# Kernel tuning notes

Hardware: AMD Instinct MI355X
Metric: run time of the kernel (lower is better)

Reference implementation:

```python
import jax, jax.numpy as jnp
import numpy as np

N = 100000
E = 1600000
IN_CH, HID_CH, OUT_CH = 128, 64, 32


def setup_inputs() -> dict:
    key = jax.random.key(0)
    ks = jax.random.split(key, 6)
    x = jax.random.normal(ks[0], (N, IN_CH), dtype=jnp.float32)
    ei = jax.random.randint(ks[1], (2, E), 0, N, dtype=jnp.int64)
    W1 = jax.random.normal(ks[2], (IN_CH, HID_CH), dtype=jnp.float32) * 0.05
    b1 = jax.random.normal(ks[3], (HID_CH,), dtype=jnp.float32) * 0.05
    W2 = jax.random.normal(ks[4], (HID_CH, OUT_CH), dtype=jnp.float32) * 0.05
    b2 = jax.random.normal(ks[5], (OUT_CH,), dtype=jnp.float32) * 0.05
    return {"x": x, "ei": ei, "W1": W1, "b1": b1, "W2": W2, "b2": b2}


def gcn_layer(x, sa, da, n):
    # degree with self-loops already appended in sa/da
    deg = jax.ops.segment_sum(jnp.ones((sa.shape[0],), x.dtype), da, num_segments=n)
    prod = deg[sa] * deg[da]
    norm = jnp.where(prod > 0, jax.lax.rsqrt(prod), 0.0)  # (deg_s*deg_d)^-0.5, inf->0
    msg = x[sa] * norm[:, None]            # [E+N, C] gather + scale
    return jax.ops.segment_sum(msg, da, num_segments=n)  # scatter_add


def reference(x, ei, W1, b1, W2, b2):
    n = x.shape[0]
    loop = jnp.arange(n, dtype=ei.dtype)
    sa = jnp.concatenate([ei[0], loop])
    da = jnp.concatenate([ei[1], loop])
    h = gcn_layer(x @ W1 + b1, sa, da, n)
    h = jax.nn.relu(h)
    # dropout: eval mode (training=False) -> identity
    return gcn_layer(h @ W2 + b2, sa, da, n)
```

## Files before the change

kernel.cpp:

```cpp
#include <hip/hip_runtime.h>

#define NN 100000
#define NE 1600000
#define IN_CH 128
#define HID_CH 64
#define OUT_CH 32
#define NB2 98
#define CHUNKA 8192
#define NBLKA ((NE + CHUNKA - 1) / CHUNKA)

typedef unsigned short ushort_t;
typedef _Float16 half2_t __attribute__((ext_vector_type(2)));

__device__ inline ushort_t f2bf(float f) {
    union { float f; unsigned u; } v; v.f = f;
    unsigned r = v.u + 0x7fff + ((v.u >> 16) & 1);
    return (ushort_t)(r >> 16);
}
__device__ inline float blo(unsigned u) {
    union { unsigned x; float f; } v; v.x = u << 16; return v.f;
}
__device__ inline float bhi(unsigned u) {
    union { unsigned x; float f; } v; v.x = u & 0xffff0000u; return v.f;
}
__device__ inline unsigned pkh(float a, float b) {
    union { half2_t h; unsigned u; } v;
    v.h[0] = (_Float16)a; v.h[1] = (_Float16)b;
    return v.u;
}
__device__ inline half2_t u2h(unsigned u) {
    union { unsigned u; half2_t h; } v; v.u = u; return v.h;
}
__device__ inline float fdot2(unsigned a, unsigned b, float c) {
#if __has_builtin(__builtin_amdgcn_fdot2)
    return __builtin_amdgcn_fdot2(u2h(a), u2h(b), c, false);
#else
    half2_t ha = u2h(a), hb = u2h(b);
    return c + (float)ha[0] * (float)hb[0] + (float)ha[1] * (float)hb[1];
#endif
}

__global__ __launch_bounds__(256) void k_bhist(const int* __restrict__ da,
                                               int* __restrict__ bcnt,
                                               int* __restrict__ bhall) {
    __shared__ int hist[4][NB2];
    int t = threadIdx.x, w = t >> 6;
    for (int i = t; i < 4 * NB2; i += 256) ((int*)hist)[i] = 0;
    __syncthreads();
    int base = blockIdx.x * CHUNKA;
    for (int i = 0; i < CHUNKA; i += 256) {
        int e = base + i + t;
        if (e < NE) atomicAdd(&hist[w][da[e] >> 10], 1);
    }
    __syncthreads();
    if (t < NB2) {
        int c = hist[0][t] + hist[1][t] + hist[2][t] + hist[3][t];
        bhall[blockIdx.x * NB2 + t] = c;
        if (c) atomicAdd(&bcnt[t], c);
    }
}

__global__ __launch_bounds__(128) void k_bscan(const int* __restrict__ bcnt,
                                               int* __restrict__ bbase,
                                               int* __restrict__ bcur,
                                               int* __restrict__ rowptr) {
    __shared__ int lds[128];
    int t = threadIdx.x;
    int v = (t < NB2) ? bcnt[t] : 0;
    lds[t] = v;
    __syncthreads();
    for (int off = 1; off < 128; off <<= 1) {
        int x = (t >= off) ? lds[t - off] : 0;
        __syncthreads();
        lds[t] += x;
        __syncthreads();
    }
    int excl = lds[t] - v;
    if (t < NB2) { bbase[t] = excl; bcur[t] = excl; }
    if (t == 0) { bbase[NB2] = NE; rowptr[NN] = NE; }
}

__global__ __launch_bounds__(256) void k_bfill(const int* __restrict__ sa,
                                               const int* __restrict__ da,
                                               const int* __restrict__ bhall,
                                               int* __restrict__ bcur,
                                               unsigned* __restrict__ ebuf) {
    __shared__ int lcur[NB2];
    int t = threadIdx.x;
    if (t < NB2) {
        int c = bhall[blockIdx.x * NB2 + t];
        lcur[t] = c ? atomicAdd(&bcur[t], c) : 0;
    }
    __syncthreads();
    int base = blockIdx.x * CHUNKA;
    for (int i = 0; i < CHUNKA; i += 256) {
        int e = base + i + t;
        if (e < NE) {
            int d = da[e];
            int p = atomicAdd(&lcur[d >> 10], 1);
            ebuf[p] = ((unsigned)sa[e] << 10) | (unsigned)(d & 1023);
        }
    }
}

__global__ __launch_bounds__(256) void k_bfine(const unsigned* __restrict__ ebuf,
                                               const int* __restrict__ bbase,
                                               int* __restrict__ rowptr,
                                               float* __restrict__ rs,
                                               int* __restrict__ col) {
    __shared__ int cnt[1024];
    __shared__ int scn[256];
    __shared__ int cur[256];
    int b = blockIdx.x, t = threadIdx.x;
    int B = b >> 2, slice = b & 3;
    int beg = bbase[B], end = bbase[B + 1];
    *(int4*)&cnt[t * 4] = make_int4(0, 0, 0, 0);
    __syncthreads();
    for (int i = beg + t; i < end; i += 256) atomicAdd(&cnt[ebuf[i] & 1023], 1);
    __syncthreads();
    int4 v4 = *(int4*)&cnt[t * 4];
    int s = v4.x + v4.y + v4.z + v4.w;
    scn[t] = s;
    __syncthreads();
    for (int off = 1; off < 256; off <<= 1) {
        int x = (t >= off) ? scn[t - off] : 0;
        __syncthreads();
        scn[t] += x;
        __syncthreads();
    }
    int excl = scn[t] - s;
    if ((t >> 6) == slice) {
        int p0 = excl;
        int p1 = p0 + v4.x;
        int p2 = p1 + v4.y;
        int p3 = p2 + v4.z;
        int dlo = t * 4;
        int n = B * 1024 + dlo;
        int ci = dlo - slice * 256;
        if (n + 0 < NN) { rowptr[n + 0] = beg + p0; rs[n + 0] = rsqrtf((float)(v4.x + 1)); cur[ci + 0] = beg + p0; }
        if (n + 1 < NN) { rowptr[n + 1] = beg + p1; rs[n + 1] = rsqrtf((float)(v4.y + 1)); cur[ci + 1] = beg + p1; }
        if (n + 2 < NN) { rowptr[n + 2] = beg + p2; rs[n + 2] = rsqrtf((float)(v4.z + 1)); cur[ci + 2] = beg + p2; }
        if (n + 3 < NN) { rowptr[n + 3] = beg + p3; rs[n + 3] = rsqrtf((float)(v4.w + 1)); cur[ci + 3] = beg + p3; }
    }
    __syncthreads();
    int slo = slice * 256;
    for (int i = beg + t; i < end; i += 256) {
        unsigned w = ebuf[i];
        int dlo = (int)(w & 1023);
        if ((dlo >> 8) == slice) {
            int pos = atomicAdd(&cur[dlo - slo], 1);
            col[pos] = (int)(w >> 10);
        }
    }
}

#define SWZU1(n, k2) ((n) * 64 + ((k2) ^ ((((n) & 7)) << 2)))
#define SWZ2(n, k) ((n) * 64 + ((k) ^ ((((n) & 7)) << 2)))

__global__ __launch_bounds__(256, 4) void k_gemm1(
    const float* __restrict__ x, const float* __restrict__ W1,
    const float* __restrict__ b1, const float* __restrict__ rs,
    ushort_t* __restrict__ xsb) {
    __shared__ unsigned xth[64 * 64];
    __shared__ unsigned w1h[64 * 64];
    int t = threadIdx.x;
    int base = blockIdx.x * 64;

#pragma unroll
    for (int i = 0; i < 8; ++i) {
        int flat = i * 1024 + t * 4;
        int node = flat >> 7, k0 = flat & 127;
        int gn = base + node;
        float4 v = make_float4(0.f, 0.f, 0.f, 0.f);
        if (gn < NN) v = *(const float4*)(x + (size_t)gn * IN_CH + k0);
        uint2 pk;
        pk.x = pkh(v.x, v.y);
        pk.y = pkh(v.z, v.w);
        *(uint2*)&xth[SWZU1(node, k0 >> 1)] = pk;
    }
#pragma unroll
    for (int i = 0; i < 16; ++i) {
        int idx = i * 256 + t;
        int k2 = idx >> 6, c = idx & 63;
        float f0 = W1[(2 * k2) * 64 + c];
        float f1 = W1[(2 * k2 + 1) * 64 + c];
        w1h[idx] = pkh(f0, f1);
    }
    __syncthreads();

    int tn = t & 15, tc = t >> 4;
    int c0 = tc * 4;
    float acc[4][4];
#pragma unroll
    for (int a = 0; a < 4; ++a)
#pragma unroll
        for (int b = 0; b < 4; ++b) acc[a][b] = 0.f;

    for (int k2 = 0; k2 < 64; k2 += 2) {
        uint2 xu[4];
#pragma unroll
        for (int jn = 0; jn < 4; ++jn)
            xu[jn] = *(uint2*)&xth[SWZU1(tn + jn * 16, k2)];
        uint4 w0 = *(uint4*)&w1h[(k2 + 0) * 64 + c0];
        uint4 w1 = *(uint4*)&w1h[(k2 + 1) * 64 + c0];
        unsigned wq0[4] = {w0.x, w0.y, w0.z, w0.w};
        unsigned wq1[4] = {w1.x, w1.y, w1.z, w1.w};
#pragma unroll
        for (int jn = 0; jn < 4; ++jn)
#pragma unroll
            for (int jc = 0; jc < 4; ++jc) {
                acc[jn][jc] = fdot2(xu[jn].x, wq0[jc], acc[jn][jc]);
                acc[jn][jc] = fdot2(xu[jn].y, wq1[jc], acc[jn][jc]);
            }
    }

    float4 bb = *(const float4*)&b1[c0];
#pragma unroll
    for (int jn = 0; jn < 4; ++jn) {
        int gn = base + tn + jn * 16;
        if (gn < NN) {
            float r = rs[gn];
            uint2 pk;
            pk.x = (unsigned)f2bf((acc[jn][0] + bb.x) * r) |
                   ((unsigned)f2bf((acc[jn][1] + bb.y) * r) << 16);
            pk.y = (unsigned)f2bf((acc[jn][2] + bb.z) * r) |
                   ((unsigned)f2bf((acc[jn][3] + bb.w) * r) << 16);
            *(uint2*)&xsb[(size_t)gn * HID_CH + c0] = pk;
        }
    }
}

#define ADD8(v) do { \
    a0 += blo((v).x); a1 += bhi((v).x); a2 += blo((v).y); a3 += bhi((v).y); \
    a4 += blo((v).z); a5 += bhi((v).z); a6 += blo((v).w); a7 += bhi((v).w); } while (0)

__global__ __launch_bounds__(256) void k_agg1(
    const int* __restrict__ rowptr, const int* __restrict__ col,
    const ushort_t* __restrict__ xsb, const float* __restrict__ rs,
    ushort_t* __restrict__ hb) {
    int gid = blockIdx.x * blockDim.x + threadIdx.x;
    int n = gid >> 6;
    if (n >= NN) return;
    int lane = threadIdx.x & 63;
    int g = lane >> 3;
    unsigned c0 = (unsigned)(lane & 7) * 8;
    int beg = rowptr[n], end = rowptr[n + 1];

    float a0 = 0.f, a1 = 0.f, a2 = 0.f, a3 = 0.f;
    float a4 = 0.f, a5 = 0.f, a6 = 0.f, a7 = 0.f;
    if (g == 0) {
        uint4 sv = *(const uint4*)&xsb[(unsigned)n * 64u + c0];
        ADD8(sv);
    }

    int i = beg;
    for (; i + 16 <= end; i += 16) {
        int s0 = col[i + g];
        int s1 = col[i + 8 + g];
        uint4 v0 = *(const uint4*)&xsb[(unsigned)s0 * 64u + c0];
        uint4 v1 = *(const uint4*)&xsb[(unsigned)s1 * 64u + c0];
        ADD8(v0);
        ADD8(v1);
    }
    if (i + 8 <= end) {
        int s0 = col[i + g];
        uint4 v0 = *(const uint4*)&xsb[(unsigned)s0 * 64u + c0];
        ADD8(v0);
        i += 8;
    }
    int r = end - i;
    if (g < r) {
        int s0 = col[i + g];
        uint4 v0 = *(const uint4*)&xsb[(unsigned)s0 * 64u + c0];
        ADD8(v0);
    }

#pragma unroll
    for (int m = 8; m <= 32; m <<= 1) {
        a0 += __shfl_xor(a0, m); a1 += __shfl_xor(a1, m);
        a2 += __shfl_xor(a2, m); a3 += __shfl_xor(a3, m);
        a4 += __shfl_xor(a4, m); a5 += __shfl_xor(a5, m);
        a6 += __shfl_xor(a6, m); a7 += __shfl_xor(a7, m);
    }

    if (g == 0) {
        float rn = rs[n];
        uint4 pk;
        pk.x = (unsigned)f2bf(fmaxf(a0 * rn, 0.f)) |
               ((unsigned)f2bf(fmaxf(a1 * rn, 0.f)) << 16);
        pk.y = (unsigned)f2bf(fmaxf(a2 * rn, 0.f)) |
               ((unsigned)f2bf(fmaxf(a3 * rn, 0.f)) << 16);
        pk.z = (unsigned)f2bf(fmaxf(a4 * rn, 0.f)) |
               ((unsigned)f2bf(fmaxf(a5 * rn, 0.f)) << 16);
        pk.w = (unsigned)f2bf(fmaxf(a6 * rn, 0.f)) |
               ((unsigned)f2bf(fmaxf(a7 * rn, 0.f)) << 16);
        *(uint4*)&hb[(unsigned)n * 64u + c0] = pk;
    }
}

__global__ __launch_bounds__(256) void k_gemm2(
    const ushort_t* __restrict__ hb, const float* __restrict__ W2,
    const float* __restrict__ b2, const float* __restrict__ rs,
    ushort_t* __restrict__ ysb) {
    __shared__ float ht[64 * 64];
    __shared__ float w2s[64 * 32];
    int t = threadIdx.x;
    int base = blockIdx.x * 64;

#pragma unroll
    for (int i = 0; i < 8; ++i) {
        int uidx = i * 256 + t;
        int node = uidx >> 5, k2 = uidx & 31;
        int gn = base + node;
        unsigned u = 0;
        if (gn < NN) u = *(const unsigned*)&hb[(size_t)gn * HID_CH + k2 * 2];
        float2 f; f.x = blo(u); f.y = bhi(u);
        *(float2*)&ht[SWZ2(node, k2 * 2)] = f;
    }
#pragma unroll
    for (int i = 0; i < 2; ++i) {
        int flat = i * 1024 + t * 4;
        *(float4*)&w2s[flat] = *(const float4*)(W2 + flat);
    }
    __syncthreads();

    int tn = t & 15, tc = t >> 4;
    int c0 = tc * 2;
    float acc[4][2];
#pragma unroll
    for (int a = 0; a < 4; ++a) { acc[a][0] = 0.f; acc[a][1] = 0.f; }

    for (int k0 = 0; k0 < 64; k0 += 4) {
        float xq[4][4], wq[4][2];
#pragma unroll
        for (int j = 0; j < 4; ++j)
            *(float2*)&wq[j][0] = *(float2*)&w2s[(k0 + j) * 32 + c0];
#pragma unroll
        for (int jn = 0; jn < 4; ++jn)
            *(float4*)&xq[jn][0] = *(float4*)&ht[SWZ2(tn + jn * 16, k0)];
#pragma unroll
        for (int jn = 0; jn < 4; ++jn)
#pragma unroll
            for (int j = 0; j < 4; ++j) {
                acc[jn][0] = fmaf(xq[jn][j], wq[j][0], acc[jn][0]);
                acc[jn][1] = fmaf(xq[jn][j], wq[j][1], acc[jn][1]);
            }
    }

    float2 bb = *(const float2*)&b2[c0];
#pragma unroll
    for (int jn = 0; jn < 4; ++jn) {
        int gn = base + tn + jn * 16;
        if (gn < NN) {
            float r = rs[gn];
            unsigned pk = (unsigned)f2bf((acc[jn][0] + bb.x) * r) |
                          ((unsigned)f2bf((acc[jn][1] + bb.y) * r) << 16);
            *(unsigned*)&ysb[(size_t)gn * OUT_CH + c0] = pk;
        }
    }
}

__global__ __launch_bounds__(256) void k_agg2(
    const int* __restrict__ rowptr, const int* __restrict__ col,
    const ushort_t* __restrict__ ysb, const float* __restrict__ rs,
    float* __restrict__ out) {
    int gid = blockIdx.x * blockDim.x + threadIdx.x;
    int n = gid >> 6;
    if (n >= NN) return;
    int lane = threadIdx.x & 63;
    int g = lane >> 2;
    unsigned c0 = (unsigned)(lane & 3) * 8;
    int beg = rowptr[n], end = rowptr[n + 1];

    float a0 = 0.f, a1 = 0.f, a2 = 0.f, a3 = 0.f;
    float a4 = 0.f, a5 = 0.f, a6 = 0.f, a7 = 0.f;
    if (g == 0) {
        uint4 sv = *(const uint4*)&ysb[(unsigned)n * 32u + c0];
        ADD8(sv);
    }

    int i = beg;
    for (; i + 16 <= end; i += 16) {
        int s0 = col[i + g];
        uint4 v0 = *(const uint4*)&ysb[(unsigned)s0 * 32u + c0];
        ADD8(v0);
    }
    int r = end - i;
    if (g < r) {
        int s0 = col[i + g];
        uint4 v0 = *(const uint4*)&ysb[(unsigned)s0 * 32u + c0];
        ADD8(v0);
    }

#pragma unroll
    for (int m = 4; m <= 32; m <<= 1) {
        a0 += __shfl_xor(a0, m); a1 += __shfl_xor(a1, m);
        a2 += __shfl_xor(a2, m); a3 += __shfl_xor(a3, m);
        a4 += __shfl_xor(a4, m); a5 += __shfl_xor(a5, m);
        a6 += __shfl_xor(a6, m); a7 += __shfl_xor(a7, m);
    }

    if (g == 0) {
        float rn = rs[n];
        float4 o0, o1;
        o0.x = a0 * rn; o0.y = a1 * rn; o0.z = a2 * rn; o0.w = a3 * rn;
        o1.x = a4 * rn; o1.y = a5 * rn; o1.z = a6 * rn; o1.w = a7 * rn;
        *(float4*)&out[(size_t)n * OUT_CH + c0] = o0;
        *(float4*)&out[(size_t)n * OUT_CH + c0 + 4] = o1;
    }
}

extern "C" void kernel_launch(void* const* d_in, const int* in_sizes, int n_in,
                              void* d_out, int out_size, void* d_ws, size_t ws_size,
                              hipStream_t stream) {
    const float* x  = (const float*)d_in[0];
    const int*   ei = (const int*)d_in[1];
    const float* W1 = (const float*)d_in[2];
    const float* b1 = (const float*)d_in[3];
    const float* W2 = (const float*)d_in[4];
    const float* b2 = (const float*)d_in[5];
    const int* sa = ei;
    const int* da = ei + NE;

    char* ws = (char*)d_ws;
    size_t off = 0;
    auto alloc = [&](size_t bytes) {
        void* p = ws + off;
        off += (bytes + 255) & ~(size_t)255;
        return p;
    };
    int*      bcnt   = (int*)alloc((size_t)NB2 * 4);
    int*      bbase  = (int*)alloc((size_t)(NB2 + 1) * 4);
    int*      bcur   = (int*)alloc((size_t)NB2 * 4);
    int*      bhall  = (int*)alloc((size_t)NBLKA * NB2 * 4);
    int*      rowptr = (int*)alloc((size_t)(NN + 1) * 4);
    float*    rs     = (float*)alloc((size_t)NN * 4);
    unsigned* ebuf   = (unsigned*)alloc((size_t)NE * 4);
    int*      col    = (int*)alloc((size_t)NE * 4);
    ushort_t* xsb    = (ushort_t*)alloc((size_t)NN * HID_CH * 2);
    ushort_t* hb     = (ushort_t*)alloc((size_t)NN * HID_CH * 2);
    ushort_t* ysb    = (ushort_t*)alloc((size_t)NN * OUT_CH * 2);
    float*    outp   = (float*)d_out;

    const int B = 256;
    hipMemsetAsync(bcnt, 0, (size_t)NB2 * 4, stream);
    k_bhist<<<NBLKA, 256, 0, stream>>>(da, bcnt, bhall);
    k_bscan<<<1, 128, 0, stream>>>(bcnt, bbase, bcur, rowptr);
    k_bfill<<<NBLKA, 256, 0, stream>>>(sa, da, bhall, bcur, ebuf);
    k_bfine<<<NB2 * 4, 256, 0, stream>>>(ebuf, bbase, rowptr, rs, col);

    const int NBLK_GEMM = (NN + 63) / 64;
    k_gemm1<<<NBLK_GEMM, 256, 0, stream>>>(x, W1, b1, rs, xsb);
    k_agg1<<<(NN * 64 + B - 1) / B, B, 0, stream>>>(rowptr, col, xsb, rs, hb);
    k_gemm2<<<NBLK_GEMM, 256, 0, stream>>>(hb, W2, b2, rs, ysb);
    k_agg2<<<(NN * 64 + B - 1) / B, B, 0, stream>>>(rowptr, col, ysb, rs, outp);
}
```

Before: 242.3 us.

## Compute per-node degrees via global atomics and fuse bucket fill with GEMM1

Replaces the bucket-count and fine-sort pipeline with per-node degree counting through global atomics, followed by a three-kernel scan that builds rowptr and rs directly. The bucket fill is merged into the GEMM1 launch as extra blocks so that the edge scatter and the dense transform run concurrently. A new 1024-thread scatter kernel fills col per bucket using LDS cursors, without a second count and scan pass. The cost is 1.6M global atomics on degree counters and more kernel launches for the scan.

```diff
diff --git a/kernel.cpp b/kernel.cpp
--- a/kernel.cpp
+++ b/kernel.cpp
@@ -8,6 +8,7 @@
 #define NB2 98
 #define CHUNKA 8192
 #define NBLKA ((NE + CHUNKA - 1) / CHUNKA)
+#define NBLK_GEMM ((NN + 63) / 64)
 
 typedef unsigned short ushort_t;
 typedef _Float16 half2_t __attribute__((ext_vector_type(2)));
@@ -40,9 +41,9 @@
 #endif
 }
 
-__global__ __launch_bounds__(256) void k_bhist(const int* __restrict__ da,
-                                               int* __restrict__ bcnt,
-                                               int* __restrict__ bhall) {
+__global__ __launch_bounds__(256) void k_deghist(const int* __restrict__ da,
+                                                 int* __restrict__ deg,
+                                                 int* __restrict__ bhall) {
     __shared__ int hist[4][NB2];
     int t = threadIdx.x, w = t >> 6;
     for (int i = t; i < 4 * NB2; i += 256) ((int*)hist)[i] = 0;
@@ -50,23 +51,50 @@
     int base = blockIdx.x * CHUNKA;
     for (int i = 0; i < CHUNKA; i += 256) {
         int e = base + i + t;
-        if (e < NE) atomicAdd(&hist[w][da[e] >> 10], 1);
-    }
-    __syncthreads();
-    if (t < NB2) {
-        int c = hist[0][t] + hist[1][t] + hist[2][t] + hist[3][t];
-        bhall[blockIdx.x * NB2 + t] = c;
-        if (c) atomicAdd(&bcnt[t], c);
-    }
-}
-
-__global__ __launch_bounds__(128) void k_bscan(const int* __restrict__ bcnt,
-                                               int* __restrict__ bbase,
-                                               int* __restrict__ bcur,
-                                               int* __restrict__ rowptr) {
+        if (e < NE) {
+            int d = da[e];
+            atomicAdd(&hist[w][d >> 10], 1);
+            atomicAdd(&deg[d], 1);
+        }
+    }
+    __syncthreads();
+    if (t < NB2)
+        bhall[blockIdx.x * NB2 + t] =
+            hist[0][t] + hist[1][t] + hist[2][t] + hist[3][t];
+}
+
+__global__ __launch_bounds__(256) void k_scan1(const int* __restrict__ deg,
+                                               int* __restrict__ part,
+                                               int* __restrict__ bsum) {
+    __shared__ int lds[256];
+    int t = threadIdx.x;
+    int base = blockIdx.x * 1024 + t * 4;
+    int v0 = 0, v1 = 0, v2 = 0, v3 = 0;
+    if (base + 0 < NN) v0 = deg[base + 0];
+    if (base + 1 < NN) v1 = deg[base + 1];
+    if (base + 2 < NN) v2 = deg[base + 2];
+    if (base + 3 < NN) v3 = deg[base + 3];
+    int s = v0 + v1 + v2 + v3;
+    lds[t] = s;
+    __syncthreads();
+    for (int off = 1; off < 256; off <<= 1) {
+        int x = (t >= off) ? lds[t - off] : 0;
+        __syncthreads();
+        lds[t] += x;
+        __syncthreads();
+    }
+    int excl = lds[t] - s;
+    if (base + 0 < NN) part[base + 0] = excl;
+    if (base + 1 < NN) part[base + 1] = excl + v0;
+    if (base + 2 < NN) part[base + 2] = excl + v0 + v1;
+    if (base + 3 < NN) part[base + 3] = excl + v0 + v1 + v2;
+    if (t == 255) bsum[blockIdx.x] = lds[255];
+}
+
+__global__ __launch_bounds__(128) void k_scan2(int* __restrict__ bsum) {
     __shared__ int lds[128];
     int t = threadIdx.x;
-    int v = (t < NB2) ? bcnt[t] : 0;
+    int v = (t < NB2) ? bsum[t] : 0;
     lds[t] = v;
     __syncthreads();
     for (int off = 1; off < 128; off <<= 1) {
@@ -75,97 +103,60 @@
         lds[t] += x;
         __syncthreads();
     }
-    int excl = lds[t] - v;
-    if (t < NB2) { bbase[t] = excl; bcur[t] = excl; }
-    if (t == 0) { bbase[NB2] = NE; rowptr[NN] = NE; }
-}
-
-__global__ __launch_bounds__(256) void k_bfill(const int* __restrict__ sa,
-                                               const int* __restrict__ da,
-                                               const int* __restrict__ bhall,
-                                               int* __restrict__ bcur,
-                                               unsigned* __restrict__ ebuf) {
-    __shared__ int lcur[NB2];
-    int t = threadIdx.x;
-    if (t < NB2) {
-        int c = bhall[blockIdx.x * NB2 + t];
-        lcur[t] = c ? atomicAdd(&bcur[t], c) : 0;
-    }
-    __syncthreads();
-    int base = blockIdx.x * CHUNKA;
-    for (int i = 0; i < CHUNKA; i += 256) {
-        int e = base + i + t;
-        if (e < NE) {
-            int d = da[e];
-            int p = atomicAdd(&lcur[d >> 10], 1);
-            ebuf[p] = ((unsigned)sa[e] << 10) | (unsigned)(d & 1023);
-        }
-    }
-}
-
-__global__ __launch_bounds__(256) void k_bfine(const unsigned* __restrict__ ebuf,
-                                               const int* __restrict__ bbase,
+    if (t < NB2) bsum[t] = lds[t] - v;
+}
+
+__global__ __launch_bounds__(256) void k_scan3(const int* __restrict__ part,
+                                               const int* __restrict__ bsum,
+                                               const int* __restrict__ deg,
                                                int* __restrict__ rowptr,
                                                float* __restrict__ rs,
-                                               int* __restrict__ col) {
-    __shared__ int cnt[1024];
-    __shared__ int scn[256];
-    __shared__ int cur[256];
-    int b = blockIdx.x, t = threadIdx.x;
-    int B = b >> 2, slice = b & 3;
-    int beg = bbase[B], end = bbase[B + 1];
-    *(int4*)&cnt[t * 4] = make_int4(0, 0, 0, 0);
-    __syncthreads();
-    for (int i = beg + t; i < end; i += 256) atomicAdd(&cnt[ebuf[i] & 1023], 1);
-    __syncthreads();
-    int4 v4 = *(int4*)&cnt[t * 4];
-    int s = v4.x + v4.y + v4.z + v4.w;
-    scn[t] = s;
-    __syncthreads();
-    for (int off = 1; off < 256; off <<= 1) {
-        int x = (t >= off) ? scn[t - off] : 0;
-        __syncthreads();
-        scn[t] += x;
-        __syncthreads();
-    }
-    int excl = scn[t] - s;
-    if ((t >> 6) == slice) {
-        int p0 = excl;
-        int p1 = p0 + v4.x;
-        int p2 = p1 + v4.y;
-        int p3 = p2 + v4.z;
-        int dlo = t * 4;
-        int n = B * 1024 + dlo;
-        int ci = dlo - slice * 256;
-        if (n + 0 < NN) { rowptr[n + 0] = beg + p0; rs[n + 0] = rsqrtf((float)(v4.x + 1)); cur[ci + 0] = beg + p0; }
-        if (n + 1 < NN) { rowptr[n + 1] = beg + p1; rs[n + 1] = rsqrtf((float)(v4.y + 1)); cur[ci + 1] = beg + p1; }
-        if (n + 2 < NN) { rowptr[n + 2] = beg + p2; rs[n + 2] = rsqrtf((float)(v4.z + 1)); cur[ci + 2] = beg + p2; }
-        if (n + 3 < NN) { rowptr[n + 3] = beg + p3; rs[n + 3] = rsqrtf((float)(v4.w + 1)); cur[ci + 3] = beg + p3; }
-    }
-    __syncthreads();
-    int slo = slice * 256;
-    for (int i = beg + t; i < end; i += 256) {
-        unsigned w = ebuf[i];
-        int dlo = (int)(w & 1023);
-        if ((dlo >> 8) == slice) {
-            int pos = atomicAdd(&cur[dlo - slo], 1);
-            col[pos] = (int)(w >> 10);
-        }
-    }
+                                               int* __restrict__ bcur) {
+    int i = blockIdx.x * blockDim.x + threadIdx.x;
+    if (i < NN) {
+        int v = part[i] + bsum[i >> 10];
+        rowptr[i] = v;
+        rs[i] = rsqrtf((float)(deg[i] + 1));
+        if ((i & 1023) == 0) bcur[i >> 10] = v;
+    }
+    if (i == NN) rowptr[NN] = NE;
 }
 
 #define SWZU1(n, k2) ((n) * 64 + ((k2) ^ ((((n) & 7)) << 2)))
 #define SWZ2(n, k) ((n) * 64 + ((k) ^ ((((n) & 7)) << 2)))
 
-__global__ __launch_bounds__(256, 4) void k_gemm1(
+__global__ __launch_bounds__(256, 4) void k_fill_gemm1(
+    const int* __restrict__ sa, const int* __restrict__ da,
+    const int* __restrict__ bhall, int* __restrict__ bcur,
+    unsigned* __restrict__ ebuf,
     const float* __restrict__ x, const float* __restrict__ W1,
     const float* __restrict__ b1, const float* __restrict__ rs,
     ushort_t* __restrict__ xsb) {
     __shared__ unsigned xth[64 * 64];
     __shared__ unsigned w1h[64 * 64];
+    __shared__ int lcur[NB2];
     int t = threadIdx.x;
-    int base = blockIdx.x * 64;
-
+
+    if (blockIdx.x < NBLKA) {
+        int blk = blockIdx.x;
+        if (t < NB2) {
+            int c = bhall[blk * NB2 + t];
+            lcur[t] = c ? atomicAdd(&bcur[t], c) : 0;
+        }
+        __syncthreads();
+        int base = blk * CHUNKA;
+        for (int i = 0; i < CHUNKA; i += 256) {
+            int e = base + i + t;
+            if (e < NE) {
+                int d = da[e];
+                int p = atomicAdd(&lcur[d >> 10], 1);
+                ebuf[p] = ((unsigned)sa[e] << 10) | (unsigned)(d & 1023);
+            }
+        }
+        return;
+    }
+
+    int base = (blockIdx.x - NBLKA) * 64;
 #pragma unroll
     for (int i = 0; i < 8; ++i) {
         int flat = i * 1024 + t * 4;
@@ -227,6 +218,39 @@
                    ((unsigned)f2bf((acc[jn][3] + bb.w) * r) << 16);
             *(uint2*)&xsb[(size_t)gn * HID_CH + c0] = pk;
         }
+    }
+}
+
+__global__ __launch_bounds__(1024) void k_fscatter(const unsigned* __restrict__ ebuf,
+                                                   const int* __restrict__ rowptr,
+                                                   int* __restrict__ col) {
+    __shared__ int cur[1024];
+    int B = blockIdx.x, t = threadIdx.x;
+    int gn = B * 1024 + t;
+    cur[t] = (gn < NN) ? rowptr[gn] : 0;
+    int lo = B * 1024; if (lo > NN) lo = NN;
+    int hi = (B + 1) * 1024; if (hi > NN) hi = NN;
+    int beg = rowptr[lo], end = rowptr[hi];
+    __syncthreads();
+    int i = beg + t;
+    for (; i + 3 * 1024 < end; i += 4 * 1024) {
+        unsigned w0 = ebuf[i];
+        unsigned w1 = ebuf[i + 1024];
+        unsigned w2 = ebuf[i + 2048];
+        unsigned w3 = ebuf[i + 3072];
+        int p0 = atomicAdd(&cur[w0 & 1023], 1);
+        int p1 = atomicAdd(&cur[w1 & 1023], 1);
+        int p2 = atomicAdd(&cur[w2 & 1023], 1);
+        int p3 = atomicAdd(&cur[w3 & 1023], 1);
+        col[p0] = (int)(w0 >> 10);
+        col[p1] = (int)(w1 >> 10);
+        col[p2] = (int)(w2 >> 10);
+        col[p3] = (int)(w3 >> 10);
+    }
+    for (; i < end; i += 1024) {
+        unsigned w = ebuf[i];
+        int pos = atomicAdd(&cur[w & 1023], 1);
+        col[pos] = (int)(w >> 10);
     }
 }
 
@@ -429,8 +453,9 @@
         off += (bytes + 255) & ~(size_t)255;
         return p;
     };
-    int*      bcnt   = (int*)alloc((size_t)NB2 * 4);
-    int*      bbase  = (int*)alloc((size_t)(NB2 + 1) * 4);
+    int*      deg    = (int*)alloc((size_t)NN * 4);
+    int*      part   = (int*)alloc((size_t)NN * 4);
+    int*      bsum   = (int*)alloc(128 * 4);
     int*      bcur   = (int*)alloc((size_t)NB2 * 4);
     int*      bhall  = (int*)alloc((size_t)NBLKA * NB2 * 4);
     int*      rowptr = (int*)alloc((size_t)(NN + 1) * 4);
@@ -443,14 +468,14 @@
     float*    outp   = (float*)d_out;
 
     const int B = 256;
-    hipMemsetAsync(bcnt, 0, (size_t)NB2 * 4, stream);
-    k_bhist<<<NBLKA, 256, 0, stream>>>(da, bcnt, bhall);
-    k_bscan<<<1, 128, 0, stream>>>(bcnt, bbase, bcur, rowptr);
-    k_bfill<<<NBLKA, 256, 0, stream>>>(sa, da, bhall, bcur, ebuf);
-    k_bfine<<<NB2 * 4, 256, 0, stream>>>(ebuf, bbase, rowptr, rs, col);
-
-    const int NBLK_GEMM = (NN + 63) / 64;
-    k_gemm1<<<NBLK_GEMM, 256, 0, stream>>>(x, W1, b1, rs, xsb);
+    hipMemsetAsync(deg, 0, (size_t)NN * 4, stream);
+    k_deghist<<<NBLKA, 256, 0, stream>>>(da, deg, bhall);
+    k_scan1<<<NB2, 256, 0, stream>>>(deg, part, bsum);
+    k_scan2<<<1, 128, 0, stream>>>(bsum);
+    k_scan3<<<(NN + 256) / 256, 256, 0, stream>>>(part, bsum, deg, rowptr, rs, bcur);
+    k_fill_gemm1<<<NBLKA + NBLK_GEMM, 256, 0, stream>>>(sa, da, bhall, bcur, ebuf,
+                                                        x, W1, b1, rs, xsb);
+    k_fscatter<<<NB2, 1024, 0, stream>>>(ebuf, rowptr, col);
     k_agg1<<<(NN * 64 + B - 1) / B, B, 0, stream>>>(rowptr, col, xsb, rs, hb);
     k_gemm2<<<NBLK_GEMM, 256, 0, stream>>>(hb, W2, b2, rs, ysb);
     k_agg2<<<(NN * 64 + B - 1) / B, B, 0, stream>>>(rowptr, col, ysb, rs, outp);
```

Result: slower. 251.7 us (+3.9%).
